# Optimization experiments

Hardware: AMD Instinct MI355X
Metric: run time of the kernel (lower is better)

## Reference

```python
import jax, jax.numpy as jnp
import numpy as np

DIM = 1024
HEADS = 16
MLP = 4096
EPS = 1e-5

def _layer_norm(x, g, b):
    mu = jnp.mean(x, axis=-1, keepdims=True)
    var = jnp.mean(jnp.square(x - mu), axis=-1, keepdims=True)
    return (x - mu) * jax.lax.rsqrt(var + EPS) * g + b

def setup_inputs() -> dict:
    key = jax.random.key(0)
    ks = jax.random.split(key, 8)
    s = 0.02
    return {
        "x": jax.random.normal(ks[0], (2, 2048, DIM), dtype=jnp.float32),
        "ln1_g": jnp.ones((DIM,), jnp.float32),
        "ln1_b": jnp.zeros((DIM,), jnp.float32),
        "qkv_w": jax.random.normal(ks[1], (DIM, 3 * DIM), jnp.float32) * s,
        "qkv_b": jnp.zeros((3 * DIM,), jnp.float32),
        "proj_w": jax.random.normal(ks[2], (DIM, DIM), jnp.float32) * s,
        "proj_b": jnp.zeros((DIM,), jnp.float32),
        "ln2_g": jnp.ones((DIM,), jnp.float32),
        "ln2_b": jnp.zeros((DIM,), jnp.float32),
        "fc1_w": jax.random.normal(ks[3], (DIM, MLP), jnp.float32) * s,
        "fc1_b": jnp.zeros((MLP,), jnp.float32),
        "fc2_w": jax.random.normal(ks[4], (MLP, DIM), jnp.float32) * s,
        "fc2_b": jnp.zeros((DIM,), jnp.float32),
    }

def reference(x, ln1_g, ln1_b, qkv_w, qkv_b, proj_w, proj_b,
              ln2_g, ln2_b, fc1_w, fc1_b, fc2_w, fc2_b):
    B, N, C = x.shape
    H = HEADS
    D = C // H
    # --- attention (pre-norm); NOTE: source applies no 1/sqrt(D) scaling ---
    h = _layer_norm(x, ln1_g, ln1_b)
    qkv = (h @ qkv_w + qkv_b).reshape(B, N, 3, H, D)
    q, k, v = (qkv[:, :, 0], qkv[:, :, 1], qkv[:, :, 2])  # [B,N,H,D]
    qk = jnp.einsum('bnhd,bmhd->bhnm', q, k)
    attn = jax.nn.softmax(qk, axis=-1)
    y = jnp.einsum('bhnm,bmhd->bnhd', attn, v).reshape(B, N, C)
    y = y @ proj_w + proj_b
    x = x + y
    # --- MLP (pre-norm), exact GELU like torch nn.GELU ---
    h2 = _layer_norm(x, ln2_g, ln2_b)
    h2 = jax.nn.gelu(h2 @ fc1_w + fc1_b, approximate=False)
    x = x + (h2 @ fc2_w + fc2_b)
    return x
```

## Files before the change

kernel.cpp:

```cpp
#include <hip/hip_runtime.h>
#include <hip/hip_bf16.h>

#define CDIM   1024
#define NSEQ   2048
#define NHEAD  16
#define HDIM   64
#define MLPDIM 4096
#define TROWS  4096

typedef __attribute__((ext_vector_type(8)))  __bf16 bf16x8;
typedef __attribute__((ext_vector_type(4)))  float  f32x4;
typedef __attribute__((ext_vector_type(16))) float  f32x16;
typedef __attribute__((ext_vector_type(4)))  unsigned short us4;

static __device__ __forceinline__ unsigned short f2bf(float f) {
  unsigned int u = __float_as_uint(f);
  u += 0x7fffu + ((u >> 16) & 1u);
  return (unsigned short)(u >> 16);
}

#define MFMA16(a, b, c) __builtin_amdgcn_mfma_f32_16x16x32_bf16(a, b, c, 0, 0, 0)
#define MFMA32(a, b, c) __builtin_amdgcn_mfma_f32_32x32x16_bf16(a, b, c, 0, 0, 0)

static __device__ __forceinline__ void gll16(const unsigned short* g, unsigned short* l) {
  __builtin_amdgcn_global_load_lds(
      (const __attribute__((address_space(1))) unsigned int*)g,
      (__attribute__((address_space(3))) unsigned int*)l, 16, 0, 0);
}

__global__ __launch_bounds__(256)
void ln_bf16_kernel(const float* __restrict__ x,
                    const float* __restrict__ gam,
                    const float* __restrict__ bet,
                    unsigned short* __restrict__ out)
{
  int row = blockIdx.x;
  int t = threadIdx.x;
  const float4* xr = (const float4*)(x + (size_t)row * CDIM);
  float4 v = xr[t];
  float s  = v.x + v.y + v.z + v.w;
  float s2 = v.x*v.x + v.y*v.y + v.z*v.z + v.w*v.w;
  #pragma unroll
  for (int off = 32; off > 0; off >>= 1) {
    s  += __shfl_down(s, off);
    s2 += __shfl_down(s2, off);
  }
  __shared__ float rs[4], rs2[4];
  int wave = t >> 6, lane = t & 63;
  if (lane == 0) { rs[wave] = s; rs2[wave] = s2; }
  __syncthreads();
  float fs  = rs[0] + rs[1] + rs[2] + rs[3];
  float fs2 = rs2[0] + rs2[1] + rs2[2] + rs2[3];
  float mu   = fs * (1.0f / CDIM);
  float var  = fs2 * (1.0f / CDIM) - mu * mu;
  float rstd = rsqrtf(var + 1e-5f);
  float4 gg = ((const float4*)gam)[t];
  float4 bb = ((const float4*)bet)[t];
  us4 o;
  o.x = f2bf((v.x - mu) * rstd * gg.x + bb.x);
  o.y = f2bf((v.y - mu) * rstd * gg.y + bb.y);
  o.z = f2bf((v.z - mu) * rstd * gg.z + bb.z);
  o.w = f2bf((v.w - mu) * rstd * gg.w + bb.w);
  ((us4*)(out + (size_t)row * CDIM))[t] = o;
}

__global__ __launch_bounds__(256)
void wt_bf16_kernel(const float* __restrict__ W, unsigned short* __restrict__ Wt,
                    int K, int N)
{
  __shared__ float tile[32][33];
  int n0 = blockIdx.x * 32, k0 = blockIdx.y * 32;
  int t = threadIdx.x;
  int r = t >> 3, c4 = (t & 7) << 2;
  float4 v = *(const float4*)(W + (size_t)(k0 + r) * N + n0 + c4);
  tile[r][c4 + 0] = v.x; tile[r][c4 + 1] = v.y;
  tile[r][c4 + 2] = v.z; tile[r][c4 + 3] = v.w;
  __syncthreads();
  us4 o;
  o.x = f2bf(tile[c4 + 0][r]);
  o.y = f2bf(tile[c4 + 1][r]);
  o.z = f2bf(tile[c4 + 2][r]);
  o.w = f2bf(tile[c4 + 3][r]);
  *(us4*)(Wt + (size_t)(n0 + r) * K + k0 + c4) = o;
}

template<int EPI>
__global__ __launch_bounds__(256, 4)
void gemm_bt(const unsigned short* __restrict__ A, const unsigned short* __restrict__ Bt,
             const float* __restrict__ bias, int Kstride, int Kc, int nbx, int nby,
             float* __restrict__ outf, unsigned short* __restrict__ outb,
             const float* __restrict__ resid, float* __restrict__ pp,
             unsigned short* __restrict__ qo, unsigned short* __restrict__ ko,
             unsigned short* __restrict__ vo)
{
  __shared__ unsigned short As[2][128 * 32];
  __shared__ unsigned short Bs[2][128 * 32];
  const int tid  = threadIdx.x;
  const int lane = tid & 63;
  const int wave = tid >> 6;
  const int wr = wave >> 1, wc = wave & 1;
  const int g = lane >> 4, r16 = lane & 15;

  const int nwg = gridDim.x;
  const int orig = ((int)blockIdx.x & 7) * (nwg >> 3) + ((int)blockIdx.x >> 3);
  const int bx = orig % nbx;
  const int t2 = orig / nbx;
  const int by = t2 % nby;
  const int kz = t2 / nby;
  const int bm = by * 128, bn = bx * 128;
  const int kbase = kz * Kc;
  const int N = nbx * 128;

  auto stage = [&](int d, int k0) {
    #pragma unroll
    for (int c = 0; c < 2; c++) {
      int o   = (c * 256 + tid) << 3;
      int row = o >> 5;
      int col = o & 31;
      int ub  = (c * 256 + (tid & ~63)) << 3;
      gll16(A  + (size_t)(bm + row) * Kstride + kbase + k0 + col, &As[d][ub]);
      gll16(Bt + (size_t)(bn + row) * Kstride + kbase + k0 + col, &Bs[d][ub]);
    }
  };

  f32x4 acc[4][4];
  #pragma unroll
  for (int i = 0; i < 4; i++)
    #pragma unroll
    for (int j = 0; j < 4; j++) acc[i][j] = (f32x4){0.f, 0.f, 0.f, 0.f};

  stage(0, 0);
  const int nkt = Kc / 32;
  for (int kt = 0; kt < nkt; kt++) {
    const int cur = kt & 1;
    __syncthreads();
    if (kt + 1 < nkt) stage(cur ^ 1, (kt + 1) * 32);
    bf16x8 af[4], bfr[4];
    #pragma unroll
    for (int i = 0; i < 4; i++) {
      int row = wr * 64 + i * 16 + r16;
      af[i] = *(const bf16x8*)(&As[cur][row * 32 + 8 * g]);
    }
    #pragma unroll
    for (int j = 0; j < 4; j++) {
      int row = wc * 64 + j * 16 + r16;
      bfr[j] = *(const bf16x8*)(&Bs[cur][row * 32 + 8 * g]);
    }
    __builtin_amdgcn_s_setprio(1);
    #pragma unroll
    for (int i = 0; i < 4; i++)
      #pragma unroll
      for (int j = 0; j < 4; j++)
        acc[i][j] = MFMA16(af[i], bfr[j], acc[i][j]);
    __builtin_amdgcn_s_setprio(0);
  }

  #pragma unroll
  for (int i = 0; i < 4; i++) {
    #pragma unroll
    for (int j = 0; j < 4; j++) {
      int col = bn + wc * 64 + j * 16 + r16;
      float bv = (EPI == 2 && kz != 0) ? 0.f : bias[col];
      #pragma unroll
      for (int jj = 0; jj < 4; jj++) {
        int row = bm + wr * 64 + i * 16 + 4 * g + jj;
        float val = acc[i][j][jj] + bv;
        if (EPI == 1) {
          int sel = col >> 10, cc = col & 1023;
          int hh = cc >> 6, d = cc & 63;
          int b = row >> 11, tk = row & 2047;
          size_t hb = (size_t)(b * NHEAD + hh);
          if (sel == 0)      qo[(hb * NSEQ + tk) * HDIM + d] = f2bf(val * 1.4426950408889634f);
          else if (sel == 1) ko[(hb * NSEQ + tk) * HDIM + d] = f2bf(val);
          else               vo[(hb * HDIM + d) * NSEQ + tk] = f2bf(val);
        } else if (EPI == 2) {
          size_t idx = (size_t)row * N + col;
          if (kz == 0) outf[idx] = val + resid[idx];
          else         pp[idx]   = val;
        } else {
          float ge = 0.5f * val * (1.0f + erff(val * 0.70710678118654752f));
          outb[(size_t)row * N + col] = f2bf(ge);
        }
      }
    }
  }
}

__global__ __launch_bounds__(256)
void add_kernel(float* __restrict__ out, const float* __restrict__ pp, int n4)
{
  int i = blockIdx.x * 256 + threadIdx.x;
  int stride = gridDim.x * 256;
  for (; i < n4; i += stride) {
    float4 a = ((const float4*)out)[i];
    float4 b = ((const float4*)pp)[i];
    a.x += b.x; a.y += b.y; a.z += b.z; a.w += b.w;
    ((float4*)out)[i] = a;
  }
}

__global__ __launch_bounds__(256, 2)
void attn_kernel(const unsigned short* __restrict__ q, const unsigned short* __restrict__ k,
                 const unsigned short* __restrict__ vt, unsigned short* __restrict__ y)
{
  int bid = blockIdx.x;
  int xcd = bid & 7, loc = bid >> 3;
  int bh  = xcd * 4 + (loc >> 4);
  int qchunk = loc & 15;
  int b = bh >> 4, h = bh & 15;
  int wave = threadIdx.x >> 6, lane = threadIdx.x & 63;
  int ql = lane & 31;
  int hi = lane >> 5;
  int q0 = qchunk * 128 + wave * 32;
  const unsigned short* qb = q  + (size_t)bh * NSEQ * HDIM;
  const unsigned short* kb = k  + (size_t)bh * NSEQ * HDIM;
  const unsigned short* vb = vt + (size_t)bh * HDIM * NSEQ;

  __shared__ unsigned short KL[2][2048];
  __shared__ unsigned short VL[2][2048];

  auto stage = [&](int d, int it) {
    int kv0 = it * 32;
    {
      int c = wave * 64 + lane;
      int row = c >> 3, col = c & 7;
      int sc  = (row << 3) | (col ^ (row & 7));
      gll16(kb + (size_t)kv0 * HDIM + sc * 8, &KL[d][wave * 512]);
    }
    {
      int c = wave * 64 + lane;
      int row = c >> 2, col = c & 3;
      int scol = col ^ ((row >> 1) & 3);
      gll16(vb + (size_t)row * NSEQ + kv0 + scol * 8, &VL[d][wave * 512]);
    }
  };

  bf16x8 aq[4];
  #pragma unroll
  for (int s = 0; s < 4; s++)
    aq[s] = *(const bf16x8*)(qb + (size_t)(q0 + ql) * HDIM + s * 16 + hi * 8);

  float ssum = 0.f;
  f32x16 o0, o1;
  #pragma unroll
  for (int r = 0; r < 16; r++) { o0[r] = 0.f; o1[r] = 0.f; }

  stage(0, 0);
  for (int it = 0; it < NSEQ / 32; it++) {
    const int cur = it & 1;
    __syncthreads();
    if (it + 1 < NSEQ / 32) stage(cur ^ 1, it + 1);
    bf16x8 kf[4];
    #pragma unroll
    for (int s = 0; s < 4; s++)
      kf[s] = *(const bf16x8*)((const char*)KL[cur] +
               ql * 128 + ((((s << 1) | hi) ^ (ql & 7)) << 4));
    f32x16 sacc;
    #pragma unroll
    for (int r = 0; r < 16; r++) sacc[r] = -32.0f;
    __builtin_amdgcn_s_setprio(1);
    #pragma unroll
    for (int s = 0; s < 4; s++)
      sacc = MFMA32(kf[s], aq[s], sacc);
    __builtin_amdgcn_s_setprio(0);
    float ps = 0.f;
    #pragma unroll
    for (int r = 0; r < 16; r++) {
      sacc[r] = exp2f(sacc[r]);
      ps += sacc[r];
    }
    ssum += ps;
    bf16x8 vf[2][2];
    #pragma unroll
    for (int t = 0; t < 2; t++)
      #pragma unroll
      for (int db = 0; db < 2; db++)
        vf[t][db] = *(const bf16x8*)((const char*)VL[cur] +
                     (db * 32 + ql) * 64 + ((((t << 1) | hi) ^ ((ql >> 1) & 3)) << 4));
    __builtin_amdgcn_s_setprio(1);
    #pragma unroll
    for (int t = 0; t < 2; t++) {
      unsigned pk01, pk23, pk45, pk67;
      asm("v_cvt_pk_bf16_f32 %0, %1, %2" : "=v"(pk01) : "v"(sacc[8*t+0]), "v"(sacc[8*t+1]));
      asm("v_cvt_pk_bf16_f32 %0, %1, %2" : "=v"(pk23) : "v"(sacc[8*t+2]), "v"(sacc[8*t+3]));
      asm("v_cvt_pk_bf16_f32 %0, %1, %2" : "=v"(pk45) : "v"(sacc[8*t+4]), "v"(sacc[8*t+5]));
      asm("v_cvt_pk_bf16_f32 %0, %1, %2" : "=v"(pk67) : "v"(sacc[8*t+6]), "v"(sacc[8*t+7]));
      asm("v_permlane32_swap_b32 %0, %1" : "+v"(pk01), "+v"(pk45));
      asm("v_permlane32_swap_b32 %0, %1" : "+v"(pk23), "+v"(pk67));
      union { unsigned u[4]; bf16x8 v; } pf;
      pf.u[0] = pk01; pf.u[1] = pk23; pf.u[2] = pk45; pf.u[3] = pk67;
      o0 = MFMA32(vf[t][0], pf.v, o0);
      o1 = MFMA32(vf[t][1], pf.v, o1);
    }
    __builtin_amdgcn_s_setprio(0);
  }
  float stot = ssum + __shfl_xor(ssum, 32);
  float inv = 1.0f / stot;
  unsigned short* yr = y + ((size_t)(b * NSEQ + q0 + ql)) * CDIM + h * HDIM;
  #pragma unroll
  for (int db = 0; db < 2; db++) {
    const f32x16& oo = db ? o1 : o0;
    #pragma unroll
    for (int rq = 0; rq < 4; rq++) {
      us4 w;
      w.x = f2bf(oo[4*rq+0] * inv);
      w.y = f2bf(oo[4*rq+1] * inv);
      w.z = f2bf(oo[4*rq+2] * inv);
      w.w = f2bf(oo[4*rq+3] * inv);
      *(us4*)(yr + db * 32 + rq * 8 + hi * 4) = w;
    }
  }
}

extern "C" void kernel_launch(void* const* d_in, const int* in_sizes, int n_in,
                              void* d_out, int out_size, void* d_ws, size_t ws_size,
                              hipStream_t stream)
{
  const float* x      = (const float*)d_in[0];
  const float* ln1_g  = (const float*)d_in[1];
  const float* ln1_b  = (const float*)d_in[2];
  const float* qkv_w  = (const float*)d_in[3];
  const float* qkv_b  = (const float*)d_in[4];
  const float* proj_w = (const float*)d_in[5];
  const float* proj_b = (const float*)d_in[6];
  const float* ln2_g  = (const float*)d_in[7];
  const float* ln2_b  = (const float*)d_in[8];
  const float* fc1_w  = (const float*)d_in[9];
  const float* fc1_b  = (const float*)d_in[10];
  const float* fc2_w  = (const float*)d_in[11];
  const float* fc2_b  = (const float*)d_in[12];
  float* out = (float*)d_out;

  char* p = (char*)d_ws;
  size_t off = 0;
  auto alloc = [&](size_t bytes) -> void* {
    void* r = p + off; off += (bytes + 255) & ~(size_t)255; return r;
  };
  unsigned short* wt_qkv  = (unsigned short*)alloc((size_t)3072 * 1024 * 2);
  unsigned short* wt_proj = (unsigned short*)alloc((size_t)1024 * 1024 * 2);
  unsigned short* wt_fc1  = (unsigned short*)alloc((size_t)4096 * 1024 * 2);
  unsigned short* wt_fc2  = (unsigned short*)alloc((size_t)1024 * 4096 * 2);
  unsigned short* h1  = (unsigned short*)alloc((size_t)TROWS * CDIM * 2);
  unsigned short* qb  = (unsigned short*)alloc((size_t)TROWS * CDIM * 2);
  unsigned short* kb  = (unsigned short*)alloc((size_t)TROWS * CDIM * 2);
  unsigned short* vtb = (unsigned short*)alloc((size_t)TROWS * CDIM * 2);
  unsigned short* yb  = (unsigned short*)alloc((size_t)TROWS * CDIM * 2);
  float*          x1  = (float*)alloc((size_t)TROWS * CDIM * 4);
  unsigned short* h2  = (unsigned short*)alloc((size_t)TROWS * CDIM * 2);
  unsigned short* g1  = (unsigned short*)alloc((size_t)TROWS * MLPDIM * 2);
  float* pp = (float*)qb;

  dim3 blk(256);
  wt_bf16_kernel<<<dim3(3072 / 32, 1024 / 32), blk, 0, stream>>>(qkv_w, wt_qkv, 1024, 3072);
  wt_bf16_kernel<<<dim3(1024 / 32, 1024 / 32), blk, 0, stream>>>(proj_w, wt_proj, 1024, 1024);
  wt_bf16_kernel<<<dim3(4096 / 32, 1024 / 32), blk, 0, stream>>>(fc1_w, wt_fc1, 1024, 4096);
  wt_bf16_kernel<<<dim3(1024 / 32, 4096 / 32), blk, 0, stream>>>(fc2_w, wt_fc2, 4096, 1024);
  ln_bf16_kernel<<<TROWS, blk, 0, stream>>>(x, ln1_g, ln1_b, h1);
  gemm_bt<1><<<dim3(768), blk, 0, stream>>>(
      h1, wt_qkv, qkv_b, 1024, 1024, 24, 32,
      nullptr, nullptr, nullptr, nullptr, qb, kb, vtb);
  attn_kernel<<<dim3(512), blk, 0, stream>>>(qb, kb, vtb, yb);
  gemm_bt<2><<<dim3(512), blk, 0, stream>>>(
      yb, wt_proj, proj_b, 1024, 512, 8, 32,
      x1, nullptr, x, pp, nullptr, nullptr, nullptr);
  add_kernel<<<dim3(2048), blk, 0, stream>>>(x1, pp, TROWS * CDIM / 4);
  ln_bf16_kernel<<<TROWS, blk, 0, stream>>>(x1, ln2_g, ln2_b, h2);
  gemm_bt<3><<<dim3(1024), blk, 0, stream>>>(
      h2, wt_fc1, fc1_b, 1024, 1024, 32, 32,
      nullptr, g1, nullptr, nullptr, nullptr, nullptr, nullptr);
  gemm_bt<2><<<dim3(512), blk, 0, stream>>>(
      g1, wt_fc2, fc2_b, 4096, 2048, 8, 32,
      out, nullptr, x1, pp, nullptr, nullptr, nullptr);
  add_kernel<<<dim3(2048), blk, 0, stream>>>(out, pp, TROWS * CDIM / 4);
}
```

Baseline: 295.4 us.

## Use 256x256 GEMM tiles for QKV and FC1, fuse split-K add into LayerNorm

Adds a 512-thread GEMM kernel with 256x256 output tiles and XOR-swizzled LDS layout, used for the QKV and FC1 projections. Each loaded tile element now feeds more MFMAs, which cuts LDS and global traffic per FLOP. The price is more accumulator registers per thread and fewer workgroups (192 and 256), which may leave some CUs underused. It also folds the split-K partial-sum add for the projection GEMM into the second LayerNorm kernel, removing one elementwise pass over the activations.

```diff
diff --git a/kernel.cpp b/kernel.cpp
--- a/kernel.cpp
+++ b/kernel.cpp
@@ -65,6 +65,45 @@
 }
 
 __global__ __launch_bounds__(256)
+void ln_add_bf16_kernel(float* __restrict__ x, const float* __restrict__ pp,
+                        const float* __restrict__ gam, const float* __restrict__ bet,
+                        unsigned short* __restrict__ out)
+{
+  int row = blockIdx.x;
+  int t = threadIdx.x;
+  float4* xr = (float4*)(x + (size_t)row * CDIM);
+  const float4* pr = (const float4*)(pp + (size_t)row * CDIM);
+  float4 v = xr[t];
+  float4 q = pr[t];
+  v.x += q.x; v.y += q.y; v.z += q.z; v.w += q.w;
+  xr[t] = v;
+  float s  = v.x + v.y + v.z + v.w;
+  float s2 = v.x*v.x + v.y*v.y + v.z*v.z + v.w*v.w;
+  #pragma unroll
+  for (int off = 32; off > 0; off >>= 1) {
+    s  += __shfl_down(s, off);
+    s2 += __shfl_down(s2, off);
+  }
+  __shared__ float rs[4], rs2[4];
+  int wave = t >> 6, lane = t & 63;
+  if (lane == 0) { rs[wave] = s; rs2[wave] = s2; }
+  __syncthreads();
+  float fs  = rs[0] + rs[1] + rs[2] + rs[3];
+  float fs2 = rs2[0] + rs2[1] + rs2[2] + rs2[3];
+  float mu   = fs * (1.0f / CDIM);
+  float var  = fs2 * (1.0f / CDIM) - mu * mu;
+  float rstd = rsqrtf(var + 1e-5f);
+  float4 gg = ((const float4*)gam)[t];
+  float4 bb = ((const float4*)bet)[t];
+  us4 o;
+  o.x = f2bf((v.x - mu) * rstd * gg.x + bb.x);
+  o.y = f2bf((v.y - mu) * rstd * gg.y + bb.y);
+  o.z = f2bf((v.z - mu) * rstd * gg.z + bb.z);
+  o.w = f2bf((v.w - mu) * rstd * gg.w + bb.w);
+  ((us4*)(out + (size_t)row * CDIM))[t] = o;
+}
+
+__global__ __launch_bounds__(256)
 void wt_bf16_kernel(const float* __restrict__ W, unsigned short* __restrict__ Wt,
                     int K, int N)
 {
@@ -85,13 +124,103 @@
 }
 
 template<int EPI>
+__global__ __launch_bounds__(512, 2)
+void gemm_bt256(const unsigned short* __restrict__ A, const unsigned short* __restrict__ Bt,
+                const float* __restrict__ bias, int Kstride, int nbx,
+                unsigned short* __restrict__ outb,
+                unsigned short* __restrict__ qo, unsigned short* __restrict__ ko,
+                unsigned short* __restrict__ vo)
+{
+  __shared__ unsigned short As[2][256 * 32];
+  __shared__ unsigned short Bs[2][256 * 32];
+  const int tid  = threadIdx.x;
+  const int lane = tid & 63;
+  const int wave = tid >> 6;
+  const int wr = wave >> 2, wc = wave & 3;
+  const int g = lane >> 4, r16 = lane & 15;
+
+  const int nwg = gridDim.x;
+  const int orig = ((int)blockIdx.x & 7) * (nwg >> 3) + ((int)blockIdx.x >> 3);
+  const int bx = orig % nbx;
+  const int by = orig / nbx;
+  const int bm = by * 256, bn = bx * 256;
+  const int N = nbx * 256;
+
+  auto stage = [&](int d, int k0) {
+    #pragma unroll
+    for (int l = 0; l < 2; l++) {
+      int c  = l * 512 + tid;
+      int sc = c ^ ((c >> 4) & 3);
+      int ub = (l * 512 + (tid & ~63)) * 8;
+      gll16(A  + (size_t)(bm + (sc >> 2)) * Kstride + k0 + ((sc & 3) << 3), &As[d][ub]);
+      gll16(Bt + (size_t)(bn + (sc >> 2)) * Kstride + k0 + ((sc & 3) << 3), &Bs[d][ub]);
+    }
+  };
+
+  f32x4 acc[8][4];
+  #pragma unroll
+  for (int i = 0; i < 8; i++)
+    #pragma unroll
+    for (int j = 0; j < 4; j++) acc[i][j] = (f32x4){0.f, 0.f, 0.f, 0.f};
+
+  stage(0, 0);
+  const int nkt = Kstride / 32;
+  for (int kt = 0; kt < nkt; kt++) {
+    const int cur = kt & 1;
+    __syncthreads();
+    if (kt + 1 < nkt) stage(cur ^ 1, (kt + 1) * 32);
+    bf16x8 af[8], bfr[4];
+    #pragma unroll
+    for (int i = 0; i < 8; i++) {
+      int row = wr * 128 + i * 16 + r16;
+      af[i] = *(const bf16x8*)(&As[cur][row * 32 + ((g ^ ((row >> 2) & 3)) << 3)]);
+    }
+    #pragma unroll
+    for (int j = 0; j < 4; j++) {
+      int row = wc * 64 + j * 16 + r16;
+      bfr[j] = *(const bf16x8*)(&Bs[cur][row * 32 + ((g ^ ((row >> 2) & 3)) << 3)]);
+    }
+    __builtin_amdgcn_s_setprio(1);
+    #pragma unroll
+    for (int i = 0; i < 8; i++)
+      #pragma unroll
+      for (int j = 0; j < 4; j++)
+        acc[i][j] = MFMA16(af[i], bfr[j], acc[i][j]);
+    __builtin_amdgcn_s_setprio(0);
+  }
+
+  #pragma unroll
+  for (int i = 0; i < 8; i++) {
+    #pragma unroll
+    for (int j = 0; j < 4; j++) {
+      int col = bn + wc * 64 + j * 16 + r16;
+      float bv = bias[col];
+      #pragma unroll
+      for (int jj = 0; jj < 4; jj++) {
+        int row = bm + wr * 128 + i * 16 + 4 * g + jj;
+        float val = acc[i][j][jj] + bv;
+        if (EPI == 1) {
+          int sel = col >> 10, cc = col & 1023;
+          int hh = cc >> 6, d = cc & 63;
+          int b = row >> 11, tk = row & 2047;
+          size_t hb = (size_t)(b * NHEAD + hh);
+          if (sel == 0)      qo[(hb * NSEQ + tk) * HDIM + d] = f2bf(val * 1.4426950408889634f);
+          else if (sel == 1) ko[(hb * NSEQ + tk) * HDIM + d] = f2bf(val);
+          else               vo[(hb * HDIM + d) * NSEQ + tk] = f2bf(val);
+        } else {
+          float ge = 0.5f * val * (1.0f + erff(val * 0.70710678118654752f));
+          outb[(size_t)row * N + col] = f2bf(ge);
+        }
+      }
+    }
+  }
+}
+
 __global__ __launch_bounds__(256, 4)
 void gemm_bt(const unsigned short* __restrict__ A, const unsigned short* __restrict__ Bt,
              const float* __restrict__ bias, int Kstride, int Kc, int nbx, int nby,
-             float* __restrict__ outf, unsigned short* __restrict__ outb,
-             const float* __restrict__ resid, float* __restrict__ pp,
-             unsigned short* __restrict__ qo, unsigned short* __restrict__ ko,
-             unsigned short* __restrict__ vo)
+             float* __restrict__ outf, const float* __restrict__ resid,
+             float* __restrict__ pp)
 {
   __shared__ unsigned short As[2][128 * 32];
   __shared__ unsigned short Bs[2][128 * 32];
@@ -160,27 +289,14 @@
     #pragma unroll
     for (int j = 0; j < 4; j++) {
       int col = bn + wc * 64 + j * 16 + r16;
-      float bv = (EPI == 2 && kz != 0) ? 0.f : bias[col];
+      float bv = (kz != 0) ? 0.f : bias[col];
       #pragma unroll
       for (int jj = 0; jj < 4; jj++) {
         int row = bm + wr * 64 + i * 16 + 4 * g + jj;
         float val = acc[i][j][jj] + bv;
-        if (EPI == 1) {
-          int sel = col >> 10, cc = col & 1023;
-          int hh = cc >> 6, d = cc & 63;
-          int b = row >> 11, tk = row & 2047;
-          size_t hb = (size_t)(b * NHEAD + hh);
-          if (sel == 0)      qo[(hb * NSEQ + tk) * HDIM + d] = f2bf(val * 1.4426950408889634f);
-          else if (sel == 1) ko[(hb * NSEQ + tk) * HDIM + d] = f2bf(val);
-          else               vo[(hb * HDIM + d) * NSEQ + tk] = f2bf(val);
-        } else if (EPI == 2) {
-          size_t idx = (size_t)row * N + col;
-          if (kz == 0) outf[idx] = val + resid[idx];
-          else         pp[idx]   = val;
-        } else {
-          float ge = 0.5f * val * (1.0f + erff(val * 0.70710678118654752f));
-          outb[(size_t)row * N + col] = f2bf(ge);
-        }
+        size_t idx = (size_t)row * N + col;
+        if (kz == 0) outf[idx] = val + resid[idx];
+        else         pp[idx]   = val;
       }
     }
   }
@@ -356,20 +472,17 @@
   wt_bf16_kernel<<<dim3(4096 / 32, 1024 / 32), blk, 0, stream>>>(fc1_w, wt_fc1, 1024, 4096);
   wt_bf16_kernel<<<dim3(1024 / 32, 4096 / 32), blk, 0, stream>>>(fc2_w, wt_fc2, 4096, 1024);
   ln_bf16_kernel<<<TROWS, blk, 0, stream>>>(x, ln1_g, ln1_b, h1);
-  gemm_bt<1><<<dim3(768), blk, 0, stream>>>(
-      h1, wt_qkv, qkv_b, 1024, 1024, 24, 32,
-      nullptr, nullptr, nullptr, nullptr, qb, kb, vtb);
+  gemm_bt256<1><<<dim3(192), dim3(512), 0, stream>>>(
+      h1, wt_qkv, qkv_b, 1024, 12, nullptr, qb, kb, vtb);
   attn_kernel<<<dim3(512), blk, 0, stream>>>(qb, kb, vtb, yb);
-  gemm_bt<2><<<dim3(512), blk, 0, stream>>>(
+  gemm_bt<<<dim3(512), blk, 0, stream>>>(
       yb, wt_proj, proj_b, 1024, 512, 8, 32,
-      x1, nullptr, x, pp, nullptr, nullptr, nullptr);
-  add_kernel<<<dim3(2048), blk, 0, stream>>>(x1, pp, TROWS * CDIM / 4);
-  ln_bf16_kernel<<<TROWS, blk, 0, stream>>>(x1, ln2_g, ln2_b, h2);
-  gemm_bt<3><<<dim3(1024), blk, 0, stream>>>(
-      h2, wt_fc1, fc1_b, 1024, 1024, 32, 32,
-      nullptr, g1, nullptr, nullptr, nullptr, nullptr, nullptr);
-  gemm_bt<2><<<dim3(512), blk, 0, stream>>>(
+      x1, x, pp);
+  ln_add_bf16_kernel<<<TROWS, blk, 0, stream>>>(x1, pp, ln2_g, ln2_b, h2);
+  gemm_bt256<3><<<dim3(256), dim3(512), 0, stream>>>(
+      h2, wt_fc1, fc1_b, 1024, 16, g1, nullptr, nullptr, nullptr);
+  gemm_bt<<<dim3(512), blk, 0, stream>>>(
       g1, wt_fc2, fc2_b, 4096, 2048, 8, 32,
-      out, nullptr, x1, pp, nullptr, nullptr, nullptr);
+      out, x1, pp);
   add_kernel<<<dim3(2048), blk, 0, stream>>>(out, pp, TROWS * CDIM / 4);
 }
```

Result: slower. 364.4 us (+23.4%).
